# Kernel tuning notes

Hardware: AMD Instinct MI355X
Metric: run time of the kernel (lower is better)

## Reference

```python
import jax, jax.numpy as jnp
import numpy as np

EMBED_DIM = 1024
NUM_HEADS = 16
HEAD_DIM = EMBED_DIM // NUM_HEADS
SCALE = HEAD_DIM ** -0.5


def setup_inputs() -> dict:
    key = jax.random.key(0)
    ks = jax.random.split(key, 9)
    B, S, D = 4, 2048, EMBED_DIM
    w_std = 1.0 / np.sqrt(D)
    x = jax.random.normal(ks[0], (B, S, D), dtype=jnp.float32)
    Wq = jax.random.uniform(ks[1], (D, D), jnp.float32, -w_std, w_std)
    bq = jax.random.uniform(ks[2], (D,), jnp.float32, -w_std, w_std)
    Wk = jax.random.uniform(ks[3], (D, D), jnp.float32, -w_std, w_std)
    bk = jax.random.uniform(ks[4], (D,), jnp.float32, -w_std, w_std)
    Wv = jax.random.uniform(ks[5], (D, D), jnp.float32, -w_std, w_std)
    bv = jax.random.uniform(ks[6], (D,), jnp.float32, -w_std, w_std)
    Wo = jax.random.uniform(ks[7], (D, D), jnp.float32, -w_std, w_std)
    bo = jax.random.uniform(ks[8], (D,), jnp.float32, -w_std, w_std)
    return {"x": x, "Wq": Wq, "bq": bq, "Wk": Wk, "bk": bk,
            "Wv": Wv, "bv": bv, "Wo": Wo, "bo": bo}


def reference(x, Wq, bq, Wk, bk, Wv, bv, Wo, bo):
    B, S, D = x.shape
    H, Dh = NUM_HEADS, HEAD_DIM
    # projections; Linear stores weight as [out,in] -> y = x @ W.T + b,
    # here W is stored as [D, D] used as x @ W + b (equivalent param'zation)
    q = (x @ Wq + bq).reshape(B, S, H, Dh).transpose(0, 2, 1, 3)  # [B,H,S,Dh]
    k = (x @ Wk + bk).reshape(B, S, H, Dh).transpose(0, 2, 1, 3)
    v = (x @ Wv + bv).reshape(B, S, H, Dh).transpose(0, 2, 1, 3)
    scores = jnp.einsum("bhqd,bhkd->bhqk", q, k) * SCALE  # [B,H,S,S]
    attn = jax.nn.softmax(scores, axis=-1)  # dropout is identity in eval mode
    out = jnp.einsum("bhqk,bhkd->bhqd", attn, v)  # [B,H,S,Dh]
    out = out.transpose(0, 2, 1, 3).reshape(B, S, D)
    return out @ Wo + bo
```

## Files before the change

### kernel.cpp

```cpp
#include <hip/hip_runtime.h>
#include <stdint.h>
#include <stddef.h>


typedef __attribute__((ext_vector_type(8)))  short          s16x8;
typedef __attribute__((ext_vector_type(8)))  unsigned short u16x8;
typedef __attribute__((ext_vector_type(4)))  unsigned short u16x4;
typedef __attribute__((ext_vector_type(4)))  float          f32x4;
typedef __attribute__((ext_vector_type(16))) float          f32x16;

#define DMODEL 1024
#define SEQ    2048
#define NHEAD  16
#define DHEAD  64
#define NTOK   8192
#define QSCALE 0.1803368801111244f

#define MFMA_B16(a, b, c) __builtin_amdgcn_mfma_f32_16x16x32_bf16((a), (b), (c), 0, 0, 0)
#define MFMA32(a, b, c)   __builtin_amdgcn_mfma_f32_32x32x16_bf16((a), (b), (c), 0, 0, 0)

__device__ __forceinline__ float bf2f(unsigned short u) {
  union { unsigned int i; float f; } v; v.i = ((unsigned int)u) << 16; return v.f;
}
__device__ __forceinline__ unsigned short f2bf(float f) {
  union { float f; unsigned int i; } v; v.f = f;
  unsigned int r = v.i + 0x7FFFu + ((v.i >> 16) & 1u);
  return (unsigned short)(r >> 16);
}
__device__ __forceinline__ float fexp2(float x) {
#if __has_builtin(__builtin_amdgcn_exp2f)
  return __builtin_amdgcn_exp2f(x);
#else
  return exp2f(x);
#endif
}
__device__ __forceinline__ unsigned int cvtpk(float a, float b) {
  unsigned int r;
  asm("v_cvt_pk_bf16_f32 %0, %1, %2" : "=v"(r) : "v"(a), "v"(b));
  return r;
}

__device__ __forceinline__ void gld16(const unsigned short* g, unsigned short* l) {
  __builtin_amdgcn_global_load_lds(
      (const __attribute__((address_space(1))) void*)g,
      (__attribute__((address_space(3))) void*)l, 16, 0, 0);
}
__device__ __forceinline__ void vmdrain() {
  asm volatile("s_waitcnt vmcnt(0)" ::: "memory");
}

__global__ void detect_fp32(const unsigned short* __restrict__ w, int* __restrict__ flag) {
  __shared__ int cnt;
  if (threadIdx.x == 0) cnt = 0;
  __syncthreads();
  int local = 0;
  for (int i = threadIdx.x; i < 8192; i += 256) {
    const unsigned short v = w[i];
    if ((v & 0x7F80u) >= 0x3F80u) local++;
  }
  atomicAdd(&cnt, local);
  __syncthreads();
  if (threadIdx.x == 0) *flag = (cnt >= 128) ? 1 : 0;
}

__global__ void norm_vec4(const void* __restrict__ s0, const void* __restrict__ s1,
                          const void* __restrict__ s2, const void* __restrict__ s3,
                          unsigned short* __restrict__ d0, unsigned short* __restrict__ d1,
                          unsigned short* __restrict__ d2, unsigned short* __restrict__ d3,
                          const int* __restrict__ flag) {
  const int fl = *flag;
  const int v = blockIdx.y;
  const void* src = (v == 0) ? s0 : (v == 1) ? s1 : (v == 2) ? s2 : s3;
  unsigned short* dst = (v == 0) ? d0 : (v == 1) ? d1 : (v == 2) ? d2 : d3;
  const int i = blockIdx.x * 256 + threadIdx.x;
  dst[i] = fl ? f2bf(((const float*)src)[i]) : ((const unsigned short*)src)[i];
}

__global__ __launch_bounds__(256) void norm_x(const void* __restrict__ src,
                                              unsigned short* __restrict__ dst,
                                              const int* __restrict__ flag) {
  const int fl = *flag;
  const size_t i = ((size_t)blockIdx.x * 256 + threadIdx.x) * 8;
  if (fl) {
    const float* s = (const float*)src + i;
    u16x8 o;
#pragma unroll
    for (int j = 0; j < 8; ++j) o[j] = f2bf(s[j]);
    *(u16x8*)(dst + i) = o;
  } else {
    *(u16x8*)(dst + i) = *(const u16x8*)((const unsigned short*)src + i);
  }
}

__global__ __launch_bounds__(256) void transpose4(const void* __restrict__ i0,
                                                  const void* __restrict__ i1,
                                                  const void* __restrict__ i2,
                                                  const void* __restrict__ i3,
                                                  unsigned short* __restrict__ o0,
                                                  unsigned short* __restrict__ o1,
                                                  unsigned short* __restrict__ o2,
                                                  unsigned short* __restrict__ o3,
                                                  const int* __restrict__ flag) {
  __shared__ unsigned short tile[64][65];
  const int z = blockIdx.z;
  const void* in = (z == 0) ? i0 : (z == 1) ? i1 : (z == 2) ? i2 : i3;
  unsigned short* out = (z == 0) ? o0 : (z == 1) ? o1 : (z == 2) ? o2 : o3;
  const int fl = *flag;
  const int tx = threadIdx.x;
  const int ty = threadIdx.y;
  const int bx = blockIdx.x * 64;
  const int by = blockIdx.y * 64;
  const float* inf = (const float*)in;
  const unsigned short* inu = (const unsigned short*)in;
#pragma unroll
  for (int i = 0; i < 16; ++i) {
    const int r = i * 4 + ty;
    const size_t idx = (size_t)(by + r) * DMODEL + bx + tx;
    tile[r][tx] = fl ? f2bf(inf[idx]) : inu[idx];
  }
  __syncthreads();
#pragma unroll
  for (int i = 0; i < 16; ++i) {
    const int r = i * 4 + ty;
    out[(size_t)(bx + r) * DMODEL + by + tx] = tile[tx][r];
  }
}

template <int MODE>
__global__ __launch_bounds__(256) void gemm_bt(const unsigned short* __restrict__ A,
                                               const unsigned short* __restrict__ Bt,
                                               const unsigned short* __restrict__ bias0,
                                               const unsigned short* __restrict__ bias1,
                                               unsigned short* __restrict__ C0,
                                               unsigned short* __restrict__ C1,
                                               void* __restrict__ Cout,
                                               const int* __restrict__ flag) {
  __shared__ __align__(16) unsigned short As[2 * 128 * 32];
  __shared__ __align__(16) unsigned short Bs[2 * 128 * 32];

  const int t = threadIdx.x;
  const int wv = t >> 6;
  const int lane = t & 63;
  const int q4 = lane >> 4;
  const int c  = lane & 15;
  const int wm = wv >> 1;
  const int wn = wv & 1;
  const int m0 = blockIdx.x * 128;
  const int n0 = blockIdx.y * 128;

  f32x4 acc[4][4];
#pragma unroll
  for (int i = 0; i < 4; ++i)
#pragma unroll
    for (int j = 0; j < 4; ++j) acc[i][j] = (f32x4){0.f, 0.f, 0.f, 0.f};

  const int ch0 = wv * 128 + lane;
  const int ch1 = ch0 + 64;
  const int ar0 = ch0 >> 2, ak0 = (ch0 & 3) * 8;
  const int ar1 = ch1 >> 2, ak1 = (ch1 & 3) * 8;

  auto aAddr = [&](int ar, int ak, int kk) -> const unsigned short* {
    if constexpr (MODE == 0) {
      const int m = m0 + ar;
      const int kc = kk + ak;
      return A + ((size_t)((m >> 11) * NHEAD + (kc >> 6)) * SEQ + (m & 2047)) * 64 +
             (kc & 63);
    } else {
      return A + (size_t)(m0 + ar) * DMODEL + ak + kk;
    }
  };
  const unsigned short* Bg0 = Bt + (size_t)(n0 + ar0) * DMODEL + ak0;
  const unsigned short* Bg1 = Bt + (size_t)(n0 + ar1) * DMODEL + ak1;
  const int lb0 = (wv * 2 + 0) * 512;
  const int lb1 = (wv * 2 + 1) * 512;

  gld16(aAddr(ar0, ak0, 0), As + lb0);
  gld16(aAddr(ar1, ak1, 0), As + lb1);
  gld16(Bg0, Bs + lb0);
  gld16(Bg1, Bs + lb1);

  for (int k0 = 0; k0 < DMODEL; k0 += 32) {
    const int cur = (k0 >> 5) & 1;
    vmdrain();
    __syncthreads();
    if (k0 + 32 < DMODEL) {
      unsigned short* Ab = As + (cur ^ 1) * 4096;
      unsigned short* Bb = Bs + (cur ^ 1) * 4096;
      gld16(aAddr(ar0, ak0, k0 + 32), Ab + lb0);
      gld16(aAddr(ar1, ak1, k0 + 32), Ab + lb1);
      gld16(Bg0 + k0 + 32, Bb + lb0);
      gld16(Bg1 + k0 + 32, Bb + lb1);
    }
    const unsigned short* Ac = As + cur * 4096;
    const unsigned short* Bc = Bs + cur * 4096;

    s16x8 af[4], bfr[4];
#pragma unroll
    for (int i = 0; i < 4; ++i)
      af[i] = *(const s16x8*)(Ac + (wm * 64 + i * 16 + c) * 32 + q4 * 8);
#pragma unroll
    for (int j = 0; j < 4; ++j)
      bfr[j] = *(const s16x8*)(Bc + (wn * 64 + j * 16 + c) * 32 + q4 * 8);
    __builtin_amdgcn_s_setprio(1);
#pragma unroll
    for (int i = 0; i < 4; ++i)
#pragma unroll
      for (int j = 0; j < 4; ++j) acc[i][j] = MFMA_B16(af[i], bfr[j], acc[i][j]);
    __builtin_amdgcn_s_setprio(0);
  }

  if (MODE == 2) {
#pragma unroll
    for (int i = 0; i < 4; ++i) {
#pragma unroll
      for (int rg = 0; rg < 4; ++rg) {
        const int m = m0 + wm * 64 + i * 16 + q4 * 4 + rg;
        const float bval = bf2f(bias0[m]);
#pragma unroll
        for (int j = 0; j < 4; ++j) {
          const int n = n0 + wn * 64 + j * 16 + c;
          C0[(((size_t)(n >> 11) * 1024 + m) << 11) + (n & 2047)] =
              f2bf(acc[i][j][rg] + bval);
        }
      }
    }
  } else if (MODE == 0) {
    const int fl = *flag;
#pragma unroll
    for (int j = 0; j < 4; ++j) {
      const int n = n0 + wn * 64 + j * 16 + c;
      const float bval = bf2f(bias0[n]);
#pragma unroll
      for (int i = 0; i < 4; ++i) {
#pragma unroll
        for (int rg = 0; rg < 4; ++rg) {
          const int m = m0 + wm * 64 + i * 16 + q4 * 4 + rg;
          const float oval = acc[i][j][rg] + bval;
          if (fl) ((float*)Cout)[(size_t)m * DMODEL + n] = oval;
          else    ((unsigned short*)Cout)[(size_t)m * DMODEL + n] = f2bf(oval);
        }
      }
    }
  } else {
#pragma unroll
    for (int j = 0; j < 4; ++j) {
      const int n = n0 + wn * 64 + j * 16 + c;
      const float bval = bf2f((n < 1024) ? bias0[n] : bias1[n & 1023]);
#pragma unroll
      for (int i = 0; i < 4; ++i) {
#pragma unroll
        for (int rg = 0; rg < 4; ++rg) {
          const int m = m0 + wm * 64 + i * 16 + q4 * 4 + rg;
          const float oval = acc[i][j][rg] + bval;
          const int d = n & 1023;
          const int h = d >> 6, dh = d & 63;
          const int b = m >> 11, s = m & 2047;
          const size_t idx = ((((size_t)b * NHEAD + h) * SEQ + s) << 6) + dh;
          if (n < 1024) C0[idx] = f2bf(oval * QSCALE);
          else          C1[idx] = f2bf(oval);
        }
      }
    }
  }
}

__global__ __launch_bounds__(256, 2) void attn_fused(const unsigned short* Qg,
                                                     const unsigned short* __restrict__ Kg,
                                                     const unsigned short* __restrict__ VTg,
                                                     unsigned short* Oq) {
  __shared__ __align__(16) unsigned short smem[16384];

  const int t = threadIdx.x;
  const int wv = t >> 6;
  const int lane = t & 63;
  const int hi = lane >> 5;
  const int ql = lane & 31;
  const int bh = blockIdx.x;
  const int q0 = blockIdx.y * 256;

  const unsigned short* Qb  = Qg  + ((size_t)bh * SEQ + q0 + wv * 64) * DHEAD;
  const unsigned short* Kb  = Kg  + (size_t)bh * SEQ * DHEAD;
  const unsigned short* VTb = VTg + (size_t)bh * DHEAD * SEQ;

  int koff[2], voff[2];
#pragma unroll
  for (int cl = 0; cl < 2; ++cl) {
    const int p = wv * 128 + cl * 64 + lane;
    const int row = p >> 3;
    const int slot = (p & 7) ^ (row & 7);
    koff[cl] = row * 64 + slot * 8;
    voff[cl] = row * 2048 + slot * 8;
  }
  int off[4];
#pragma unroll
  for (int s = 0; s < 4; ++s) off[s] = (((s * 2 + hi) ^ (ql & 7)) * 8);

  {
    unsigned short* Kd = smem;
    unsigned short* Vd = smem + 4096;
#pragma unroll
    for (int cl = 0; cl < 2; ++cl) {
      gld16(Kb + koff[cl], Kd + (wv * 128 + cl * 64) * 8);
      gld16(VTb + voff[cl], Vd + (wv * 128 + cl * 64) * 8);
    }
  }

  s16x8 qf[2][4];
#pragma unroll
  for (int qt = 0; qt < 2; ++qt)
#pragma unroll
    for (int s = 0; s < 4; ++s)
      qf[qt][s] = *(const s16x8*)(Qb + (size_t)(qt * 32 + ql) * DHEAD + s * 16 + hi * 8);

  f32x16 acco[2][2];
#pragma unroll
  for (int qt = 0; qt < 2; ++qt)
#pragma unroll
    for (int dt = 0; dt < 2; ++dt)
#pragma unroll
      for (int r = 0; r < 16; ++r) acco[qt][dt][r] = 0.f;
  f32x16 zv;
#pragma unroll
  for (int r = 0; r < 16; ++r) zv[r] = 0.f;
  float rs[2][4] = {{0.f, 0.f, 0.f, 0.f}, {0.f, 0.f, 0.f, 0.f}};

  for (int kt = 0; kt < SEQ / 64; ++kt) {
    vmdrain();
    __syncthreads();
    const int cur = kt & 1;
    if (kt + 1 < SEQ / 64) {
      unsigned short* Kd = smem + (cur ^ 1) * 8192;
      unsigned short* Vd = smem + (cur ^ 1) * 8192 + 4096;
      const unsigned short* Ksrc = Kb + (size_t)(kt + 1) * 64 * DHEAD;
      const unsigned short* Vsrc = VTb + (size_t)(kt + 1) * 64;
#pragma unroll
      for (int cl = 0; cl < 2; ++cl) {
        gld16(Ksrc + koff[cl], Kd + (wv * 128 + cl * 64) * 8);
        gld16(Vsrc + voff[cl], Vd + (wv * 128 + cl * 64) * 8);
      }
    }
    const unsigned short* Ksb = smem + cur * 8192;
    const unsigned short* Vtb = smem + cur * 8192 + 4096;

    f32x16 accs[2][2];
    __builtin_amdgcn_s_setprio(1);
#pragma unroll
    for (int k2 = 0; k2 < 2; ++k2) {
#pragma unroll
      for (int s = 0; s < 4; ++s) {
        const s16x8 kf = *(const s16x8*)(Ksb + (k2 * 32 + ql) * 64 + off[s]);
        if (s == 0) {
          accs[0][k2] = MFMA32(kf, qf[0][s], zv);
          accs[1][k2] = MFMA32(kf, qf[1][s], zv);
        } else {
          accs[0][k2] = MFMA32(kf, qf[0][s], accs[0][k2]);
          accs[1][k2] = MFMA32(kf, qf[1][s], accs[1][k2]);
        }
      }
    }
    __builtin_amdgcn_s_setprio(0);

    unsigned int u[2][2][8];
#pragma unroll
    for (int qt = 0; qt < 2; ++qt) {
#pragma unroll
      for (int k2 = 0; k2 < 2; ++k2) {
#pragma unroll
        for (int r = 0; r < 16; ++r) {
          const float p = fexp2(accs[qt][k2][r]);
          accs[qt][k2][r] = p;
          rs[qt][r & 3] += p;
        }
#pragma unroll
        for (int i = 0; i < 8; ++i)
          u[qt][k2][i] = cvtpk(accs[qt][k2][2 * i], accs[qt][k2][2 * i + 1]);
      }
    }

    __builtin_amdgcn_s_setprio(1);
#pragma unroll
    for (int k2 = 0; k2 < 2; ++k2) {
#pragma unroll
      for (int s = 0; s < 2; ++s) {
        const int kap = k2 * 2 + s;
        const s16x8 vf0 = *(const s16x8*)(Vtb + (0 * 32 + ql) * 64 + off[kap]);
        const s16x8 vf1 = *(const s16x8*)(Vtb + (1 * 32 + ql) * 64 + off[kap]);
#pragma unroll
        for (int qt = 0; qt < 2; ++qt) {
          unsigned int a0 = u[qt][k2][4 * s + 0], b0 = u[qt][k2][4 * s + 2];
          unsigned int a1 = u[qt][k2][4 * s + 1], b1 = u[qt][k2][4 * s + 3];
          asm("v_permlane32_swap_b32 %0, %1" : "+v"(a0), "+v"(b0));
          asm("v_permlane32_swap_b32 %0, %1" : "+v"(a1), "+v"(b1));
          union { unsigned int w[4]; s16x8 v; } pb;
          pb.w[0] = a0; pb.w[1] = a1; pb.w[2] = b0; pb.w[3] = b1;
          acco[qt][0] = MFMA32(vf0, pb.v, acco[qt][0]);
          acco[qt][1] = MFMA32(vf1, pb.v, acco[qt][1]);
        }
      }
    }
    __builtin_amdgcn_s_setprio(0);
  }

#pragma unroll
  for (int qt = 0; qt < 2; ++qt) {
    float lsum = (rs[qt][0] + rs[qt][1]) + (rs[qt][2] + rs[qt][3]);
    lsum += __shfl_xor(lsum, 32);
    const float inv = 1.0f / lsum;
    const int tok = q0 + wv * 64 + qt * 32 + ql;
    unsigned short* orow = Oq + ((size_t)bh * SEQ + tok) * DHEAD;
#pragma unroll
    for (int dt = 0; dt < 2; ++dt) {
#pragma unroll
      for (int rq = 0; rq < 4; ++rq) {
        u16x4 o;
#pragma unroll
        for (int j = 0; j < 4; ++j) o[j] = f2bf(acco[qt][dt][rq * 4 + j] * inv);
        *(u16x4*)(orow + dt * 32 + rq * 8 + hi * 4) = o;
      }
    }
  }
}

extern "C" void kernel_launch(void* const* d_in, const int* in_sizes, int n_in,
                              void* d_out, int out_size, void* d_ws, size_t ws_size,
                              hipStream_t stream) {
  const void* x  = d_in[0];
  const void* Wq = d_in[1];
  const void* bq = d_in[2];
  const void* Wk = d_in[3];
  const void* bk = d_in[4];
  const void* Wv = d_in[5];
  const void* bv = d_in[6];
  const void* Wo = d_in[7];
  const void* bo = d_in[8];

  unsigned short* ws = (unsigned short*)d_ws;
  const size_t M1 = (size_t)DMODEL * DMODEL;
  const size_t MQ = (size_t)NTOK * DMODEL;

  unsigned short* Qw  = ws;
  unsigned short* Kw  = Qw + MQ;
  unsigned short* Vw  = Kw + MQ;
  unsigned short* WqT = Vw + MQ;
  unsigned short* WkT = WqT + M1;
  unsigned short* WvT = WkT + M1;
  unsigned short* WoT = WvT + M1;
  unsigned short* bqn = WoT + M1;
  unsigned short* bkn = bqn + 1024;
  unsigned short* bvn = bkn + 1024;
  unsigned short* bon = bvn + 1024;
  int*            flg = (int*)(bon + 1024);
  unsigned short* Xb  = (unsigned short*)d_out;

  detect_fp32<<<1, 256, 0, stream>>>((const unsigned short*)Wq, flg);

  norm_vec4<<<dim3(4, 4), 256, 0, stream>>>(bq, bk, bv, bo,
                                            bqn, bkn, bvn, bon, flg);

  transpose4<<<dim3(16, 16, 4), dim3(64, 4), 0, stream>>>(
      Wq, Wk, Wv, Wo, WqT, WkT, WvT, WoT, flg);

  norm_x<<<4096, 256, 0, stream>>>(x, Xb, flg);

  gemm_bt<1><<<dim3(64, 16), 256, 0, stream>>>(Xb, WqT, bqn, bkn, Qw, Kw,
                                               nullptr, nullptr);
  gemm_bt<2><<<dim3(8, 64), 256, 0, stream>>>(WvT, Xb, bvn, nullptr, Vw, nullptr,
                                              nullptr, nullptr);

  attn_fused<<<dim3(64, 8), 256, 0, stream>>>(Qw, Kw, Vw, Qw);

  gemm_bt<0><<<dim3(64, 8), 256, 0, stream>>>(Qw, WoT, bon, nullptr,
                                              nullptr, nullptr, d_out, flg);
}
```

Before: 288.7 us.

## Split attention block into 8 waves of 32 queries each

The attention kernel now launches 512 threads per block, with each of the 8 waves handling 32 query rows instead of 64. Each wave also loads one K/V chunk per tile instead of two. This halves per-wave accumulator and register state, which allows higher occupancy (launch bounds 512,4) and more waves to hide latency. In exchange, each K/V fragment read from LDS feeds half as many MFMAs, so LDS traffic per FLOP doubles, and the larger block synchronises more waves per barrier.

```diff
diff --git a/kernel.cpp b/kernel.cpp
--- a/kernel.cpp
+++ b/kernel.cpp
@@ -264,7 +264,7 @@
   }
 }
 
-__global__ __launch_bounds__(256, 2) void attn_fused(const unsigned short* Qg,
+__global__ __launch_bounds__(512, 4) void attn_fused(const unsigned short* Qg,
                                                      const unsigned short* __restrict__ Kg,
                                                      const unsigned short* __restrict__ VTg,
                                                      unsigned short* Oq) {
@@ -278,103 +278,77 @@
   const int bh = blockIdx.x;
   const int q0 = blockIdx.y * 256;
 
-  const unsigned short* Qb  = Qg  + ((size_t)bh * SEQ + q0 + wv * 64) * DHEAD;
+  const unsigned short* Qb  = Qg  + ((size_t)bh * SEQ + q0 + wv * 32) * DHEAD;
   const unsigned short* Kb  = Kg  + (size_t)bh * SEQ * DHEAD;
   const unsigned short* VTb = VTg + (size_t)bh * DHEAD * SEQ;
 
-  int koff[2], voff[2];
-#pragma unroll
-  for (int cl = 0; cl < 2; ++cl) {
-    const int p = wv * 128 + cl * 64 + lane;
+  int koff, voff;
+  {
+    const int p = wv * 64 + lane;
     const int row = p >> 3;
     const int slot = (p & 7) ^ (row & 7);
-    koff[cl] = row * 64 + slot * 8;
-    voff[cl] = row * 2048 + slot * 8;
+    koff = row * 64 + slot * 8;
+    voff = row * 2048 + slot * 8;
   }
   int off[4];
 #pragma unroll
   for (int s = 0; s < 4; ++s) off[s] = (((s * 2 + hi) ^ (ql & 7)) * 8);
 
-  {
-    unsigned short* Kd = smem;
-    unsigned short* Vd = smem + 4096;
-#pragma unroll
-    for (int cl = 0; cl < 2; ++cl) {
-      gld16(Kb + koff[cl], Kd + (wv * 128 + cl * 64) * 8);
-      gld16(VTb + voff[cl], Vd + (wv * 128 + cl * 64) * 8);
-    }
-  }
-
-  s16x8 qf[2][4];
-#pragma unroll
-  for (int qt = 0; qt < 2; ++qt)
-#pragma unroll
-    for (int s = 0; s < 4; ++s)
-      qf[qt][s] = *(const s16x8*)(Qb + (size_t)(qt * 32 + ql) * DHEAD + s * 16 + hi * 8);
-
-  f32x16 acco[2][2];
-#pragma unroll
-  for (int qt = 0; qt < 2; ++qt)
-#pragma unroll
-    for (int dt = 0; dt < 2; ++dt)
-#pragma unroll
-      for (int r = 0; r < 16; ++r) acco[qt][dt][r] = 0.f;
+  gld16(Kb + koff, smem + wv * 512);
+  gld16(VTb + voff, smem + 4096 + wv * 512);
+
+  s16x8 qf[4];
+#pragma unroll
+  for (int s = 0; s < 4; ++s)
+    qf[s] = *(const s16x8*)(Qb + (size_t)ql * DHEAD + s * 16 + hi * 8);
+
+  f32x16 acco[2];
+#pragma unroll
+  for (int dt = 0; dt < 2; ++dt)
+#pragma unroll
+    for (int r = 0; r < 16; ++r) acco[dt][r] = 0.f;
   f32x16 zv;
 #pragma unroll
   for (int r = 0; r < 16; ++r) zv[r] = 0.f;
-  float rs[2][4] = {{0.f, 0.f, 0.f, 0.f}, {0.f, 0.f, 0.f, 0.f}};
+  float rs[4] = {0.f, 0.f, 0.f, 0.f};
 
   for (int kt = 0; kt < SEQ / 64; ++kt) {
     vmdrain();
     __syncthreads();
     const int cur = kt & 1;
     if (kt + 1 < SEQ / 64) {
-      unsigned short* Kd = smem + (cur ^ 1) * 8192;
-      unsigned short* Vd = smem + (cur ^ 1) * 8192 + 4096;
-      const unsigned short* Ksrc = Kb + (size_t)(kt + 1) * 64 * DHEAD;
-      const unsigned short* Vsrc = VTb + (size_t)(kt + 1) * 64;
-#pragma unroll
-      for (int cl = 0; cl < 2; ++cl) {
-        gld16(Ksrc + koff[cl], Kd + (wv * 128 + cl * 64) * 8);
-        gld16(Vsrc + voff[cl], Vd + (wv * 128 + cl * 64) * 8);
-      }
+      gld16(Kb + (size_t)(kt + 1) * 64 * DHEAD + koff,
+            smem + (cur ^ 1) * 8192 + wv * 512);
+      gld16(VTb + (size_t)(kt + 1) * 64 + voff,
+            smem + (cur ^ 1) * 8192 + 4096 + wv * 512);
     }
     const unsigned short* Ksb = smem + cur * 8192;
     const unsigned short* Vtb = smem + cur * 8192 + 4096;
 
-    f32x16 accs[2][2];
+    f32x16 accs[2];
     __builtin_amdgcn_s_setprio(1);
 #pragma unroll
     for (int k2 = 0; k2 < 2; ++k2) {
 #pragma unroll
       for (int s = 0; s < 4; ++s) {
         const s16x8 kf = *(const s16x8*)(Ksb + (k2 * 32 + ql) * 64 + off[s]);
-        if (s == 0) {
-          accs[0][k2] = MFMA32(kf, qf[0][s], zv);
-          accs[1][k2] = MFMA32(kf, qf[1][s], zv);
-        } else {
-          accs[0][k2] = MFMA32(kf, qf[0][s], accs[0][k2]);
-          accs[1][k2] = MFMA32(kf, qf[1][s], accs[1][k2]);
-        }
+        accs[k2] = MFMA32(kf, qf[s], (s == 0) ? zv : accs[k2]);
       }
     }
     __builtin_amdgcn_s_setprio(0);
 
-    unsigned int u[2][2][8];
-#pragma unroll
-    for (int qt = 0; qt < 2; ++qt) {
-#pragma unroll
-      for (int k2 = 0; k2 < 2; ++k2) {
-#pragma unroll
-        for (int r = 0; r < 16; ++r) {
-          const float p = fexp2(accs[qt][k2][r]);
-          accs[qt][k2][r] = p;
-          rs[qt][r & 3] += p;
-        }
-#pragma unroll
-        for (int i = 0; i < 8; ++i)
-          u[qt][k2][i] = cvtpk(accs[qt][k2][2 * i], accs[qt][k2][2 * i + 1]);
-      }
+    unsigned int u[2][8];
+#pragma unroll
+    for (int k2 = 0; k2 < 2; ++k2) {
+#pragma unroll
+      for (int r = 0; r < 16; ++r) {
+        const float p = fexp2(accs[k2][r]);
+        accs[k2][r] = p;
+        rs[r & 3] += p;
+      }
+#pragma unroll
+      for (int i = 0; i < 8; ++i)
+        u[k2][i] = cvtpk(accs[k2][2 * i], accs[k2][2 * i + 1]);
     }
 
     __builtin_amdgcn_s_setprio(1);
@@ -385,38 +359,32 @@
         const int kap = k2 * 2 + s;
         const s16x8 vf0 = *(const s16x8*)(Vtb + (0 * 32 + ql) * 64 + off[kap]);
         const s16x8 vf1 = *(const s16x8*)(Vtb + (1 * 32 + ql) * 64 + off[kap]);
-#pragma unroll
-        for (int qt = 0; qt < 2; ++qt) {
-          unsigned int a0 = u[qt][k2][4 * s + 0], b0 = u[qt][k2][4 * s + 2];
-          unsigned int a1 = u[qt][k2][4 * s + 1], b1 = u[qt][k2][4 * s + 3];
-          asm("v_permlane32_swap_b32 %0, %1" : "+v"(a0), "+v"(b0));
-          asm("v_permlane32_swap_b32 %0, %1" : "+v"(a1), "+v"(b1));
-          union { unsigned int w[4]; s16x8 v; } pb;
-          pb.w[0] = a0; pb.w[1] = a1; pb.w[2] = b0; pb.w[3] = b1;
-          acco[qt][0] = MFMA32(vf0, pb.v, acco[qt][0]);
-          acco[qt][1] = MFMA32(vf1, pb.v, acco[qt][1]);
-        }
+        unsigned int a0 = u[k2][4 * s + 0], b0 = u[k2][4 * s + 2];
+        unsigned int a1 = u[k2][4 * s + 1], b1 = u[k2][4 * s + 3];
+        asm("v_permlane32_swap_b32 %0, %1" : "+v"(a0), "+v"(b0));
+        asm("v_permlane32_swap_b32 %0, %1" : "+v"(a1), "+v"(b1));
+        union { unsigned int w[4]; s16x8 v; } pb;
+        pb.w[0] = a0; pb.w[1] = a1; pb.w[2] = b0; pb.w[3] = b1;
+        acco[0] = MFMA32(vf0, pb.v, acco[0]);
+        acco[1] = MFMA32(vf1, pb.v, acco[1]);
       }
     }
     __builtin_amdgcn_s_setprio(0);
   }
 
-#pragma unroll
-  for (int qt = 0; qt < 2; ++qt) {
-    float lsum = (rs[qt][0] + rs[qt][1]) + (rs[qt][2] + rs[qt][3]);
-    lsum += __shfl_xor(lsum, 32);
-    const float inv = 1.0f / lsum;
-    const int tok = q0 + wv * 64 + qt * 32 + ql;
-    unsigned short* orow = Oq + ((size_t)bh * SEQ + tok) * DHEAD;
-#pragma unroll
-    for (int dt = 0; dt < 2; ++dt) {
-#pragma unroll
-      for (int rq = 0; rq < 4; ++rq) {
-        u16x4 o;
-#pragma unroll
-        for (int j = 0; j < 4; ++j) o[j] = f2bf(acco[qt][dt][rq * 4 + j] * inv);
-        *(u16x4*)(orow + dt * 32 + rq * 8 + hi * 4) = o;
-      }
+  float lsum = (rs[0] + rs[1]) + (rs[2] + rs[3]);
+  lsum += __shfl_xor(lsum, 32);
+  const float inv = 1.0f / lsum;
+  const int tok = q0 + wv * 32 + ql;
+  unsigned short* orow = Oq + ((size_t)bh * SEQ + tok) * DHEAD;
+#pragma unroll
+  for (int dt = 0; dt < 2; ++dt) {
+#pragma unroll
+    for (int rq = 0; rq < 4; ++rq) {
+      u16x4 o;
+#pragma unroll
+      for (int j = 0; j < 4; ++j) o[j] = f2bf(acco[dt][rq * 4 + j] * inv);
+      *(u16x4*)(orow + dt * 32 + rq * 8 + hi * 4) = o;
     }
   }
 }
@@ -467,7 +435,7 @@
   gemm_bt<2><<<dim3(8, 64), 256, 0, stream>>>(WvT, Xb, bvn, nullptr, Vw, nullptr,
                                               nullptr, nullptr);
 
-  attn_fused<<<dim3(64, 8), 256, 0, stream>>>(Qw, Kw, Vw, Qw);
+  attn_fused<<<dim3(64, 8), 512, 0, stream>>>(Qw, Kw, Vw, Qw);
 
   gemm_bt<0><<<dim3(64, 8), 256, 0, stream>>>(Qw, WoT, bon, nullptr,
                                               nullptr, nullptr, d_out, flg);
```

Result: slower. 318.6 us (+10.3%).
